# Optimization experiments

Measured on AMD Instinct MI355X. Metric: run time of the kernel, lower is better.

Reference implementation:

```python
import jax, jax.numpy as jnp
import numpy as np

TOP_K = 8
ROUTED_SCALING_FACTOR = 1.0
EPS = 1e-20


def setup_inputs() -> dict:
    key = jax.random.key(0)
    k1, k2, k3 = jax.random.split(key, 3)
    T, D, E = 8192, 4096, 64
    x = jax.random.normal(k1, (T, D), dtype=jnp.float32)
    gate_weight = jax.random.normal(k2, (E, D), dtype=jnp.float32) * (1.0 / np.sqrt(D))
    bias = jax.random.normal(k3, (E,), dtype=jnp.float32) * 0.1
    return {"x": x, "gate_weight": gate_weight, "bias": bias}


def reference(x, gate_weight, bias):
    # logits: [T, E] = x [T, D] @ gate_weight.T [D, E]
    logits = jnp.einsum('td,ed->te', x.astype(jnp.float32), gate_weight)
    scores = jax.nn.sigmoid(logits)
    biased = scores + bias  # broadcast [E]
    # top-k on biased scores, sorted descending
    _, indices = jax.lax.top_k(biased, TOP_K)  # [T, K]
    selected_scores = jnp.take_along_axis(scores, indices, axis=-1)  # [T, K]
    normalized = selected_scores / (jnp.sum(selected_scores, axis=-1, keepdims=True) + EPS)
    weights = normalized * ROUTED_SCALING_FACTOR
    return (indices, weights)
```

## Files before the change

### kernel.cpp

```cpp
#include <hip/hip_runtime.h>
#include <math.h>

#define T_TOK 8192
#define DDIM  4096
#define NEXP  64
#define TOPK  8

typedef __attribute__((ext_vector_type(8))) _Float16 half8;
typedef __attribute__((ext_vector_type(4))) float f32x4;

#define RS 2048.0f

__global__ __launch_bounds__(256) void pack_w(
    const float* __restrict__ gw, _Float16* __restrict__ wpk)
{
    const int g    = blockIdx.x * 256 + threadIdx.x;
    const int lane = g & 63;
    const int n    = (g >> 6) & 3;
    const int kt   = g >> 8;
    const int e    = n * 16 + (lane & 15);
    const int k    = kt * 32 + (lane >> 4) * 8;

    const float* src = gw + (size_t)e * DDIM + k;
    float4 v0 = *reinterpret_cast<const float4*>(src);
    float4 v1 = *reinterpret_cast<const float4*>(src + 4);
    const float v[8] = {v0.x, v0.y, v0.z, v0.w, v1.x, v1.y, v1.z, v1.w};

    half8 h0, h1;
    #pragma unroll
    for (int j = 0; j < 8; j++) {
        _Float16 a = (_Float16)v[j];
        h0[j] = a;
        h1[j] = (_Float16)((v[j] - (float)a) * RS);
    }
    size_t base = ((size_t)(kt * 4 + n) * 2) * 512;
    *reinterpret_cast<half8*>(wpk + base + lane * 8)       = h0;
    *reinterpret_cast<half8*>(wpk + base + 512 + lane * 8) = h1;
}

template<int S>
__global__ __launch_bounds__(256, 2) void gemm_part(
    const float* __restrict__ x, const _Float16* __restrict__ wpk,
    float* __restrict__ part)
{
    constexpr int STEPS = 128 / S;
    const int lane = threadIdx.x & 63;
    const int wv   = threadIdx.x >> 6;
    const int slc  = blockIdx.x >> 6;
    const int pair = ((blockIdx.x & 63) << 2) | wv;
    const int tok0 = pair * 32;
    const int am   = lane & 15;
    const int ag   = lane >> 4;

    const float* xr0 = x + (size_t)(tok0 + am) * DDIM + slc * (DDIM / S) + ag * 8;
    const float* xr1 = xr0 + (size_t)16 * DDIM;
    const _Float16* bbase = wpk + (size_t)slc * STEPS * 8 * 512 + lane * 8;

    f32x4 aH[2][4], aM[2][4];
    #pragma unroll
    for (int t = 0; t < 2; t++)
        #pragma unroll
        for (int n = 0; n < 4; n++) {
            aH[t][n] = (f32x4){0.f, 0.f, 0.f, 0.f};
            aM[t][n] = (f32x4){0.f, 0.f, 0.f, 0.f};
        }

    float4 av[3][4];
    half8  bf[2][8];

    #pragma unroll
    for (int st = 0; st < 2; st++) {
        av[st][0] = *reinterpret_cast<const float4*>(xr0 + st * 32);
        av[st][1] = *reinterpret_cast<const float4*>(xr0 + st * 32 + 4);
        av[st][2] = *reinterpret_cast<const float4*>(xr1 + st * 32);
        av[st][3] = *reinterpret_cast<const float4*>(xr1 + st * 32 + 4);
    }
    #pragma unroll
    for (int n = 0; n < 4; n++) {
        bf[0][2 * n]     = *reinterpret_cast<const half8*>(bbase + n * 1024);
        bf[0][2 * n + 1] = *reinterpret_cast<const half8*>(bbase + n * 1024 + 512);
    }

    #pragma unroll
    for (int st = 0; st < STEPS; st++) {
        const int cur  = st & 1;
        const int nxt  = cur ^ 1;
        const int acur = st % 3;

        if (st + 2 < STEPS) {
            const int ap = (st + 2) % 3;
            av[ap][0] = *reinterpret_cast<const float4*>(xr0 + (st + 2) * 32);
            av[ap][1] = *reinterpret_cast<const float4*>(xr0 + (st + 2) * 32 + 4);
            av[ap][2] = *reinterpret_cast<const float4*>(xr1 + (st + 2) * 32);
            av[ap][3] = *reinterpret_cast<const float4*>(xr1 + (st + 2) * 32 + 4);
        }
        if (st + 1 < STEPS) {
            const _Float16* bp = bbase + (size_t)(st + 1) * 8 * 512;
            #pragma unroll
            for (int n = 0; n < 4; n++) {
                bf[nxt][2 * n]     = *reinterpret_cast<const half8*>(bp + n * 1024);
                bf[nxt][2 * n + 1] = *reinterpret_cast<const half8*>(bp + n * 1024 + 512);
            }
        }

        half8 a0[2], a1[2];
        #pragma unroll
        for (int t = 0; t < 2; t++) {
            const float* vv = reinterpret_cast<const float*>(&av[acur][2 * t]);
            #pragma unroll
            for (int j = 0; j < 8; j++) {
                float v = vv[j];
                _Float16 h = (_Float16)v;
                a0[t][j] = h;
                a1[t][j] = (_Float16)((v - (float)h) * RS);
            }
        }
        #pragma unroll
        for (int t = 0; t < 2; t++)
            #pragma unroll
            for (int n = 0; n < 4; n++) {
                aH[t][n] = __builtin_amdgcn_mfma_f32_16x16x32_f16(a0[t], bf[cur][2 * n],     aH[t][n], 0, 0, 0);
                aM[t][n] = __builtin_amdgcn_mfma_f32_16x16x32_f16(a0[t], bf[cur][2 * n + 1], aM[t][n], 0, 0, 0);
                aM[t][n] = __builtin_amdgcn_mfma_f32_16x16x32_f16(a1[t], bf[cur][2 * n],     aM[t][n], 0, 0, 0);
            }
    }

    const float i1 = 1.0f / RS;
    float* po = part + (size_t)slc * T_TOK * NEXP + (size_t)tok0 * NEXP;
    #pragma unroll
    for (int t = 0; t < 2; t++)
        #pragma unroll
        for (int n = 0; n < 4; n++)
            #pragma unroll
            for (int r = 0; r < 4; r++) {
                float vv = aH[t][n][r] + aM[t][n][r] * i1;
                po[(size_t)(t * 16 + ag * 4 + r) * NEXP + n * 16 + am] = vv;
            }
}

__global__ __launch_bounds__(256) void reduce_topk(
    const float* __restrict__ part, const float* __restrict__ bias,
    float* __restrict__ out, int S)
{
    const int wave = threadIdx.x >> 6;
    const int lane = threadIdx.x & 63;
    const int j    = blockIdx.x;
    const int g    = j & 7;
    const int q    = j >> 3;
    const int token = g * 128 + (q & 31) * 4 + (q >> 5) * 1024 + wave;
    if (token >= T_TOK) return;

    float logit = 0.f;
    for (int s = 0; s < S; s++)
        logit += part[(size_t)s * T_TOK * NEXP + (size_t)token * NEXP + lane];

    float score  = 1.f / (1.f + expf(-logit));
    float biased = score + bias[lane];

    float my_sc = 0.f;
    int   my_idx = 0;
    float ssum  = 0.f;

    #pragma unroll
    for (int jj = 0; jj < TOPK; jj++) {
        float v = biased;
        int   i = lane;
        #pragma unroll
        for (int off = 32; off >= 1; off >>= 1) {
            float ov = __shfl_xor(v, off);
            int   oi = __shfl_xor(i, off);
            if (ov > v || (ov == v && oi < i)) { v = ov; i = oi; }
        }
        float s_sel = __shfl(score, i);
        ssum += s_sel;
        if (lane == jj) { my_idx = i; my_sc = s_sel; }
        if (lane == i) biased = -INFINITY;
    }

    if (lane < TOPK) {
        out[(size_t)token * TOPK + lane] = (float)my_idx;
        out[(size_t)T_TOK * TOPK + (size_t)token * TOPK + lane]
            = my_sc / (ssum + 1e-20f);
    }
}

extern "C" void kernel_launch(void* const* d_in, const int* in_sizes, int n_in,
                              void* d_out, int out_size, void* d_ws, size_t ws_size,
                              hipStream_t stream) {
    (void)in_sizes; (void)n_in; (void)out_size;
    const float* x    = (const float*)d_in[0];
    const float* gw   = (const float*)d_in[1];
    const float* bias = (const float*)d_in[2];
    float* out = (float*)d_out;
    _Float16* wpk = (_Float16*)d_ws;
    float* part = (float*)(wpk + (size_t)DDIM * NEXP * 2);

    const size_t wpk_bytes = (size_t)DDIM * NEXP * 2 * sizeof(_Float16);
    const size_t per_slice = (size_t)T_TOK * NEXP * sizeof(float);
    int S = 1;
    for (int cand : {8, 4, 2}) {
        if (wpk_bytes + (size_t)cand * per_slice <= ws_size) { S = cand; break; }
    }

    pack_w<<<128, 256, 0, stream>>>(gw, wpk);

    dim3 b1(256);
    switch (S) {
        case 8: gemm_part<8><<<dim3(64 * 8), b1, 0, stream>>>(x, wpk, part); break;
        case 4: gemm_part<4><<<dim3(64 * 4), b1, 0, stream>>>(x, wpk, part); break;
        case 2: gemm_part<2><<<dim3(64 * 2), b1, 0, stream>>>(x, wpk, part); break;
        default: gemm_part<1><<<dim3(64), b1, 0, stream>>>(x, wpk, part); break;
    }

    reduce_topk<<<dim3(T_TOK / 4), 256, 0, stream>>>(part, bias, out, S);
}
```

Measured before the change: 53.92 us.

## Fuse split-K GEMM and top-k into one kernel with LDS reduction

Replaces the split-K GEMM that wrote partial logits to global memory, and the separate reduce/top-k kernel, with one kernel. Each 512-thread block handles 32 tokens, and its 8 waves each take one K slice. Partials are summed in shared memory, then each wave runs sigmoid and top-k for 4 tokens. This removes the global partial-sum round trip and one kernel launch. In exchange there are 256 blocks using 64KB of LDS each, which may lower occupancy and latency hiding.

```diff
diff --git a/kernel.cpp b/kernel.cpp
--- a/kernel.cpp
+++ b/kernel.cpp
@@ -5,6 +5,8 @@
 #define DDIM  4096
 #define NEXP  64
 #define TOPK  8
+#define WAVES 8
+#define STEPS 16
 
 typedef __attribute__((ext_vector_type(8))) _Float16 half8;
 typedef __attribute__((ext_vector_type(4))) float f32x4;
@@ -38,23 +40,22 @@
     *reinterpret_cast<half8*>(wpk + base + 512 + lane * 8) = h1;
 }
 
-template<int S>
-__global__ __launch_bounds__(256, 2) void gemm_part(
+__global__ __launch_bounds__(512, 2) void gemm_topk(
     const float* __restrict__ x, const _Float16* __restrict__ wpk,
-    float* __restrict__ part)
+    const float* __restrict__ bias, float* __restrict__ out)
 {
-    constexpr int STEPS = 128 / S;
-    const int lane = threadIdx.x & 63;
-    const int wv   = threadIdx.x >> 6;
-    const int slc  = blockIdx.x >> 6;
-    const int pair = ((blockIdx.x & 63) << 2) | wv;
-    const int tok0 = pair * 32;
+    __shared__ float red[WAVES][32][NEXP];
+
+    const int tid  = threadIdx.x;
+    const int lane = tid & 63;
+    const int wv   = tid >> 6;
+    const int tok0 = blockIdx.x * 32;
     const int am   = lane & 15;
     const int ag   = lane >> 4;
 
-    const float* xr0 = x + (size_t)(tok0 + am) * DDIM + slc * (DDIM / S) + ag * 8;
+    const float* xr0 = x + (size_t)(tok0 + am) * DDIM + wv * (DDIM / WAVES) + ag * 8;
     const float* xr1 = xr0 + (size_t)16 * DDIM;
-    const _Float16* bbase = wpk + (size_t)slc * STEPS * 8 * 512 + lane * 8;
+    const _Float16* bbase = wpk + (size_t)(wv * STEPS) * 8 * 512 + lane * 8;
 
     f32x4 aH[2][4], aM[2][4];
     #pragma unroll
@@ -126,91 +127,69 @@
     }
 
     const float i1 = 1.0f / RS;
-    float* po = part + (size_t)slc * T_TOK * NEXP + (size_t)tok0 * NEXP;
     #pragma unroll
     for (int t = 0; t < 2; t++)
         #pragma unroll
         for (int n = 0; n < 4; n++)
             #pragma unroll
-            for (int r = 0; r < 4; r++) {
-                float vv = aH[t][n][r] + aM[t][n][r] * i1;
-                po[(size_t)(t * 16 + ag * 4 + r) * NEXP + n * 16 + am] = vv;
+            for (int r = 0; r < 4; r++)
+                red[wv][t * 16 + ag * 4 + r][n * 16 + am]
+                    = aH[t][n][r] + aM[t][n][r] * i1;
+    __syncthreads();
+
+    {
+        const int tok = tid >> 4;
+        const int c4  = tid & 15;
+        float4 s0 = *reinterpret_cast<const float4*>(&red[0][tok][c4 * 4]);
+        #pragma unroll
+        for (int s = 1; s < WAVES; s++) {
+            float4 v = *reinterpret_cast<const float4*>(&red[s][tok][c4 * 4]);
+            s0.x += v.x; s0.y += v.y; s0.z += v.z; s0.w += v.w;
+        }
+        *reinterpret_cast<float4*>(&red[0][tok][c4 * 4]) = s0;
+    }
+    __syncthreads();
+
+    const float bsv = bias[lane];
+    #pragma unroll
+    for (int ti = 0; ti < 4; ti++) {
+        const int tk = wv * 4 + ti;
+        float logit  = red[0][tk][lane];
+        float score  = 1.f / (1.f + expf(-logit));
+        float biased = score + bsv;
+        float my_sc = 0.f; int my_idx = 0; float ssum = 0.f;
+        #pragma unroll
+        for (int j = 0; j < TOPK; j++) {
+            float vb = biased; int ib = lane;
+            #pragma unroll
+            for (int off = 32; off >= 1; off >>= 1) {
+                float ov = __shfl_xor(vb, off);
+                int   oi = __shfl_xor(ib, off);
+                if (ov > vb || (ov == vb && oi < ib)) { vb = ov; ib = oi; }
             }
-}
-
-__global__ __launch_bounds__(256) void reduce_topk(
-    const float* __restrict__ part, const float* __restrict__ bias,
-    float* __restrict__ out, int S)
-{
-    const int wave = threadIdx.x >> 6;
-    const int lane = threadIdx.x & 63;
-    const int j    = blockIdx.x;
-    const int g    = j & 7;
-    const int q    = j >> 3;
-    const int token = g * 128 + (q & 31) * 4 + (q >> 5) * 1024 + wave;
-    if (token >= T_TOK) return;
-
-    float logit = 0.f;
-    for (int s = 0; s < S; s++)
-        logit += part[(size_t)s * T_TOK * NEXP + (size_t)token * NEXP + lane];
-
-    float score  = 1.f / (1.f + expf(-logit));
-    float biased = score + bias[lane];
-
-    float my_sc = 0.f;
-    int   my_idx = 0;
-    float ssum  = 0.f;
-
-    #pragma unroll
-    for (int jj = 0; jj < TOPK; jj++) {
-        float v = biased;
-        int   i = lane;
-        #pragma unroll
-        for (int off = 32; off >= 1; off >>= 1) {
-            float ov = __shfl_xor(v, off);
-            int   oi = __shfl_xor(i, off);
-            if (ov > v || (ov == v && oi < i)) { v = ov; i = oi; }
+            float s_sel = __shfl(score, ib);
+            ssum += s_sel;
+            if (lane == j) { my_idx = ib; my_sc = s_sel; }
+            if (lane == ib) biased = -INFINITY;
         }
-        float s_sel = __shfl(score, i);
-        ssum += s_sel;
-        if (lane == jj) { my_idx = i; my_sc = s_sel; }
-        if (lane == i) biased = -INFINITY;
-    }
-
-    if (lane < TOPK) {
-        out[(size_t)token * TOPK + lane] = (float)my_idx;
-        out[(size_t)T_TOK * TOPK + (size_t)token * TOPK + lane]
-            = my_sc / (ssum + 1e-20f);
+        if (lane < TOPK) {
+            out[(size_t)(tok0 + tk) * TOPK + lane] = (float)my_idx;
+            out[(size_t)T_TOK * TOPK + (size_t)(tok0 + tk) * TOPK + lane]
+                = my_sc / (ssum + 1e-20f);
+        }
     }
 }
 
 extern "C" void kernel_launch(void* const* d_in, const int* in_sizes, int n_in,
                               void* d_out, int out_size, void* d_ws, size_t ws_size,
                               hipStream_t stream) {
-    (void)in_sizes; (void)n_in; (void)out_size;
+    (void)in_sizes; (void)n_in; (void)out_size; (void)ws_size;
     const float* x    = (const float*)d_in[0];
     const float* gw   = (const float*)d_in[1];
     const float* bias = (const float*)d_in[2];
     float* out = (float*)d_out;
     _Float16* wpk = (_Float16*)d_ws;
-    float* part = (float*)(wpk + (size_t)DDIM * NEXP * 2);
-
-    const size_t wpk_bytes = (size_t)DDIM * NEXP * 2 * sizeof(_Float16);
-    const size_t per_slice = (size_t)T_TOK * NEXP * sizeof(float);
-    int S = 1;
-    for (int cand : {8, 4, 2}) {
-        if (wpk_bytes + (size_t)cand * per_slice <= ws_size) { S = cand; break; }
-    }
 
     pack_w<<<128, 256, 0, stream>>>(gw, wpk);
-
-    dim3 b1(256);
-    switch (S) {
-        case 8: gemm_part<8><<<dim3(64 * 8), b1, 0, stream>>>(x, wpk, part); break;
-        case 4: gemm_part<4><<<dim3(64 * 4), b1, 0, stream>>>(x, wpk, part); break;
-        case 2: gemm_part<2><<<dim3(64 * 2), b1, 0, stream>>>(x, wpk, part); break;
-        default: gemm_part<1><<<dim3(64), b1, 0, stream>>>(x, wpk, part); break;
-    }
-
-    reduce_topk<<<dim3(T_TOK / 4), 256, 0, stream>>>(part, bias, out, S);
+    gemm_topk<<<T_TOK / 32, 512, 0, stream>>>(x, wpk, bias, out);
 }
```

Measured after the change: 54.56 us. No clear change (+1.2%).
